# Kernel tuning notes

Hardware: AMD Instinct MI355X
Metric: run time of the kernel (lower is better)

## Reference

```python
import jax, jax.numpy as jnp
import numpy as np

BATCH = 8192
HIDDEN = 512
VOCAB = 128
SEQ_LEN = 128  # loop runs SEQ_LEN - 1 steps


def setup_inputs() -> dict:
    key = jax.random.key(0)
    ks = jax.random.split(key, 9)
    s_ih = 1.0 / np.sqrt(HIDDEN)
    inp = {
        "z": jax.random.normal(ks[0], (BATCH, HIDDEN), dtype=jnp.float32),
        # nn.LSTMCell params (gate order: i, f, g, o)
        "W_ih": jax.random.uniform(ks[1], (4 * HIDDEN, VOCAB), jnp.float32, -s_ih, s_ih),
        "W_hh": jax.random.uniform(ks[2], (4 * HIDDEN, HIDDEN), jnp.float32, -s_ih, s_ih),
        "b_ih": jax.random.uniform(ks[3], (4 * HIDDEN,), jnp.float32, -s_ih, s_ih),
        "b_hh": jax.random.uniform(ks[4], (4 * HIDDEN,), jnp.float32, -s_ih, s_ih),
        # cell_state_from_z: Linear(hidden, hidden)
        "W_cz": jax.random.uniform(ks[5], (HIDDEN, HIDDEN), jnp.float32, -s_ih, s_ih),
        "b_cz": jax.random.uniform(ks[6], (HIDDEN,), jnp.float32, -s_ih, s_ih),
        # fc: Linear(hidden, vocab)
        "W_fc": jax.random.uniform(ks[7], (VOCAB, HIDDEN), jnp.float32, -s_ih, s_ih),
        "b_fc": jax.random.uniform(ks[8], (VOCAB,), jnp.float32, -s_ih, s_ih),
    }
    return inp


def reference(z, W_ih, W_hh, b_ih, b_hh, W_cz, b_cz, W_fc, b_fc):
    batch = z.shape[0]
    # learnable cell state from z
    c0 = jax.nn.relu(z @ W_cz.T + b_cz)
    h0 = z
    # start token: one-hot at index 0
    tok0 = jnp.zeros((batch, VOCAB), dtype=z.dtype).at[:, 0].set(1.0)
    b = b_ih + b_hh

    def step(carry, _):
        h, c, tok = carry
        gates = tok @ W_ih.T + h @ W_hh.T + b  # (batch, 4H)
        i, f, g, o = jnp.split(gates, 4, axis=-1)
        i = jax.nn.sigmoid(i)
        f = jax.nn.sigmoid(f)
        g = jnp.tanh(g)
        o = jax.nn.sigmoid(o)
        c_new = f * c + i * g
        h_new = o * jnp.tanh(c_new)
        logits = jax.nn.relu(h_new @ W_fc.T + b_fc)  # (batch, vocab)
        # softmax then argmax == argmax of logits; feed one-hot of greedy token
        tok_new = jax.nn.one_hot(jnp.argmax(logits, axis=-1), VOCAB, dtype=z.dtype)
        return (h_new, c_new, tok_new), logits

    _, out = jax.lax.scan(step, (h0, c0, tok0), None, length=SEQ_LEN - 1)
    return jnp.transpose(out, (1, 0, 2))  # (batch, seq_len-1, vocab)
```

## Files before the change

### kernel.cpp

```cpp
#include <hip/hip_runtime.h>
#include <math.h>
#include <stdint.h>

#define BATCH  8192
#define HIDDEN 512
#define VOCAB  128
#define NSTEP  127
#define OUTROW (NSTEP * VOCAB)
#define NG     2048

using half8   = __attribute__((ext_vector_type(8))) _Float16;
using half4   = __attribute__((ext_vector_type(4))) _Float16;
using float4v = __attribute__((ext_vector_type(4))) float;

#define GLD16(g, l) __builtin_amdgcn_global_load_lds( \
    (const __attribute__((address_space(1))) void*)(g), \
    (__attribute__((address_space(3))) void*)(l), 16, 0, 0)

__device__ __forceinline__ float fast_rcp(float x) { return __builtin_amdgcn_rcpf(x); }
__device__ __forceinline__ float fast_sig(float x) { return fast_rcp(1.0f + __expf(-x)); }
__device__ __forceinline__ float fast_tanh(float x) { return 1.0f - 2.0f * fast_rcp(1.0f + __expf(2.0f * x)); }

__device__ __forceinline__ int orig_row_of(int np) {
    int bn = np >> 7, cc = np & 127;
    int wv = cc >> 6, cw = cc & 63;
    int gate = cw >> 4, jjl = cw & 15;
    int jj = bn * 32 + wv * 16 + jjl;
    return gate * HIDDEN + jj;
}

__global__ __launch_bounds__(256) void init_tok_kernel(int* __restrict__ tok) {
    int i = blockIdx.x * 256 + threadIdx.x;
    if (i < BATCH) tok[i] = 0;
}

__global__ __launch_bounds__(256) void prep_whh_kernel(
    const float* __restrict__ Whh, _Float16* __restrict__ wh, _Float16* __restrict__ wl)
{
    int np = blockIdx.x;
    int orig = orig_row_of(np);
    for (int k = threadIdx.x; k < HIDDEN; k += 256) {
        float w = Whh[(size_t)orig * HIDDEN + k] * 2048.0f;
        _Float16 h = (_Float16)w;
        wh[(size_t)np * HIDDEN + k] = h;
        wl[(size_t)np * HIDDEN + k] = (_Float16)(w - (float)h);
    }
}

__global__ __launch_bounds__(128) void prep_wih_kernel(
    const float* __restrict__ Wih, const float* __restrict__ bih,
    const float* __restrict__ bhh, float* __restrict__ wihT, float* __restrict__ bcomb)
{
    int np = blockIdx.x;
    int orig = orig_row_of(np);
    int v = threadIdx.x;
    wihT[(size_t)v * NG + np] = Wih[(size_t)orig * VOCAB + v];
    if (v == 0) bcomb[np] = bih[orig] + bhh[orig];
}

__global__ __launch_bounds__(256) void prep_wfc_kernel(
    const float* __restrict__ Wfc, _Float16* __restrict__ wh, _Float16* __restrict__ wl)
{
    int i = blockIdx.x * 256 + threadIdx.x;
    float w = Wfc[i] * 2048.0f;
    _Float16 h = (_Float16)w;
    wh[i] = h;
    wl[i] = (_Float16)(w - (float)h);
}

__global__ __launch_bounds__(256) void prep_z_kernel(
    const float* __restrict__ z, _Float16* __restrict__ zh, _Float16* __restrict__ zl)
{
    int i = blockIdx.x * 256 + threadIdx.x;
    float4 v = ((const float4*)z)[i];
    float s0 = v.x * 2048.f, s1 = v.y * 2048.f, s2 = v.z * 2048.f, s3 = v.w * 2048.f;
    _Float16 h0 = (_Float16)s0, h1 = (_Float16)s1, h2 = (_Float16)s2, h3 = (_Float16)s3;
    half4 H = {h0, h1, h2, h3};
    half4 L = {(_Float16)(s0 - (float)h0), (_Float16)(s1 - (float)h1),
               (_Float16)(s2 - (float)h2), (_Float16)(s3 - (float)h3)};
    ((half4*)zh)[i] = H;
    ((half4*)zl)[i] = L;
}

__global__ __launch_bounds__(256) void c0_kernel(
    const float* __restrict__ z, const float* __restrict__ Wcz,
    const float* __restrict__ bcz, float* __restrict__ c)
{
    __shared__ float As[16][128];
    __shared__ float Bs[16][128];
    const int m0 = blockIdx.x * 128;
    const int n0 = blockIdx.y * 128;
    const int tid = threadIdx.x;
    const int ty = tid >> 4, tx = tid & 15;

    float acc[8][8];
#pragma unroll
    for (int i = 0; i < 8; ++i)
#pragma unroll
        for (int j = 0; j < 8; ++j) acc[i][j] = 0.f;

    for (int kc = 0; kc < HIDDEN; kc += 16) {
#pragma unroll
        for (int i = 0; i < 2; ++i) {
            int id = tid * 2 + i;
            int row = id >> 2;
            int kq = (id & 3) * 4;
            float4 av = *(const float4*)(z + (size_t)(m0 + row) * HIDDEN + kc + kq);
            As[kq + 0][row] = av.x; As[kq + 1][row] = av.y;
            As[kq + 2][row] = av.z; As[kq + 3][row] = av.w;
            float4 bv = *(const float4*)(Wcz + (size_t)(n0 + row) * HIDDEN + kc + kq);
            Bs[kq + 0][row] = bv.x; Bs[kq + 1][row] = bv.y;
            Bs[kq + 2][row] = bv.z; Bs[kq + 3][row] = bv.w;
        }
        __syncthreads();
#pragma unroll 4
        for (int k = 0; k < 16; ++k) {
            float a[8], b[8];
            *(float4*)&a[0] = *(const float4*)&As[k][ty * 8];
            *(float4*)&a[4] = *(const float4*)&As[k][ty * 8 + 4];
            *(float4*)&b[0] = *(const float4*)&Bs[k][tx * 8];
            *(float4*)&b[4] = *(const float4*)&Bs[k][tx * 8 + 4];
#pragma unroll
            for (int i = 0; i < 8; ++i)
#pragma unroll
                for (int j = 0; j < 8; ++j)
                    acc[i][j] = fmaf(a[i], b[j], acc[i][j]);
        }
        __syncthreads();
    }
#pragma unroll
    for (int i = 0; i < 8; ++i) {
        int m = m0 + ty * 8 + i;
#pragma unroll
        for (int j = 0; j < 8; ++j) {
            int n = n0 + tx * 8 + j;
            c[(size_t)m * HIDDEN + n] = fmaxf(acc[i][j] + bcz[n], 0.f);
        }
    }
}

__global__ __launch_bounds__(512, 2) void lstm_mfma_kernel(
    const _Float16* __restrict__ hin_h, const _Float16* __restrict__ hin_l,
    const _Float16* __restrict__ whh_h, const _Float16* __restrict__ whh_l,
    const float* __restrict__ wihT, const float* __restrict__ bcomb,
    const int* __restrict__ tok, float* __restrict__ c,
    _Float16* __restrict__ hout_h, _Float16* __restrict__ hout_l)
{
    __shared__ _Float16 Ah_s[2][256][32];
    __shared__ _Float16 Al_s[2][256][32];
    __shared__ _Float16 Bh_s[2][256][32];
    __shared__ _Float16 Bl_s[2][256][32];

    const int tid  = threadIdx.x;
    const int wid  = tid >> 6, lane = tid & 63;
    const int wr   = wid >> 2, wc = wid & 3;
    const int m0   = blockIdx.x * 256;
    const int n0   = blockIdx.y * 256;

    float4v acc[8][4];
#pragma unroll
    for (int i = 0; i < 8; ++i)
#pragma unroll
        for (int j = 0; j < 4; ++j) acc[i][j] = (float4v){0.f, 0.f, 0.f, 0.f};

    const int lrow = lane >> 2;
    const int lchk = (lane & 3) ^ ((lane >> 3) & 3);
    const int loff = lrow * HIDDEN + lchk * 8;
    const int base = wid * 32;

    const _Float16* agh = hin_h + (size_t)(m0 + base) * HIDDEN + loff;
    const _Float16* agl = hin_l + (size_t)(m0 + base) * HIDDEN + loff;
    const _Float16* bgh = whh_h + (size_t)(n0 + base) * HIDDEN + loff;
    const _Float16* bgl = whh_l + (size_t)(n0 + base) * HIDDEN + loff;

    auto STAGE = [&](int buf, int kc) {
        GLD16(agh + kc,               &Ah_s[buf][base][0]);
        GLD16(agh + kc + 16 * HIDDEN, &Ah_s[buf][base + 16][0]);
        GLD16(agl + kc,               &Al_s[buf][base][0]);
        GLD16(agl + kc + 16 * HIDDEN, &Al_s[buf][base + 16][0]);
        GLD16(bgh + kc,               &Bh_s[buf][base][0]);
        GLD16(bgh + kc + 16 * HIDDEN, &Bh_s[buf][base + 16][0]);
        GLD16(bgl + kc,               &Bl_s[buf][base][0]);
        GLD16(bgl + kc + 16 * HIDDEN, &Bl_s[buf][base + 16][0]);
    };

    const int t = lane & 15, qr = lane >> 4;
    const int qa = (qr ^ ((t >> 1) & 3)) * 8;

    STAGE(0, 0);
    for (int k = 0; k < 16; ++k) {
        const int cur = k & 1;
        if (k < 15) STAGE(cur ^ 1, (k + 1) * 32);
        if (k < 15) { asm volatile("s_waitcnt vmcnt(8)" ::: "memory"); }
        else        { asm volatile("s_waitcnt vmcnt(0)" ::: "memory"); }
        __builtin_amdgcn_s_barrier();
        __builtin_amdgcn_sched_barrier(0);

        {
            const _Float16 (*AhC)[32] = Ah_s[cur];
            const _Float16 (*AlC)[32] = Al_s[cur];
            const _Float16 (*BhC)[32] = Bh_s[cur];
            const _Float16 (*BlC)[32] = Bl_s[cur];
            half8 bh[4], bl[4];
#pragma unroll
            for (int j = 0; j < 4; ++j) {
                bh[j] = *(const half8*)&BhC[wc * 64 + j * 16 + t][qa];
                bl[j] = *(const half8*)&BlC[wc * 64 + j * 16 + t][qa];
            }
#pragma unroll
            for (int i = 0; i < 8; ++i) {
                half8 ah = *(const half8*)&AhC[wr * 128 + i * 16 + t][qa];
                half8 al = *(const half8*)&AlC[wr * 128 + i * 16 + t][qa];
#pragma unroll
                for (int j = 0; j < 4; ++j) {
                    acc[i][j] = __builtin_amdgcn_mfma_f32_16x16x32_f16(ah, bh[j], acc[i][j], 0, 0, 0);
                    acc[i][j] = __builtin_amdgcn_mfma_f32_16x16x32_f16(ah, bl[j], acc[i][j], 0, 0, 0);
                    acc[i][j] = __builtin_amdgcn_mfma_f32_16x16x32_f16(al, bh[j], acc[i][j], 0, 0, 0);
                }
            }
        }
        __builtin_amdgcn_sched_barrier(0);
        if (k < 15) {
            asm volatile("" ::: "memory");
            __builtin_amdgcn_s_barrier();
        }
    }

    const float INV22 = 1.0f / 4194304.0f;
    const int g  = blockIdx.y * 4 + wc;
    const int jj = (g >> 1) * 32 + (g & 1) * 16 + t;
    const int colb = n0 + wc * 64 + t;
    float bias[4];
    int   col[4];
#pragma unroll
    for (int j = 0; j < 4; ++j) {
        col[j]  = colb + j * 16;
        bias[j] = bcomb[col[j]];
    }
#pragma unroll
    for (int i = 0; i < 8; ++i) {
        int mb = m0 + wr * 128 + i * 16 + qr * 4;
#pragma unroll
        for (int r = 0; r < 4; ++r) {
            int m  = mb + r;
            int tk = tok[m];
            const float* wv = wihT + (size_t)tk * NG;
            float iv = acc[i][0][r] * INV22 + bias[0] + wv[col[0]];
            float fv = acc[i][1][r] * INV22 + bias[1] + wv[col[1]];
            float gv = acc[i][2][r] * INV22 + bias[2] + wv[col[2]];
            float ov = acc[i][3][r] * INV22 + bias[3] + wv[col[3]];
            float ig = fast_sig(iv);
            float fg = fast_sig(fv);
            float gg = fast_tanh(gv);
            float og = fast_sig(ov);
            size_t ci = (size_t)m * HIDDEN + jj;
            float cn = fg * c[ci] + ig * gg;
            c[ci] = cn;
            float hn = og * fast_tanh(cn);
            float hs = hn * 2048.f;
            _Float16 hh = (_Float16)hs;
            hout_h[ci] = hh;
            hout_l[ci] = (_Float16)(hs - (float)hh);
        }
    }
}

__global__ __launch_bounds__(128) void logits_mfma_kernel(
    const _Float16* __restrict__ hh_, const _Float16* __restrict__ hl_,
    const _Float16* __restrict__ wfc_h, const _Float16* __restrict__ wfc_l,
    const float* __restrict__ b_fc, float* __restrict__ out_t, int* __restrict__ tok)
{
    __shared__ _Float16 Ah[32][64];
    __shared__ _Float16 Al[32][64];
    __shared__ _Float16 Bh[128][64];
    __shared__ _Float16 Bl[128][64];

    const int tid = threadIdx.x;
    const int wid = tid >> 6, lane = tid & 63;
    const int m0  = blockIdx.x * 32;
    const int t   = lane & 15, qr = lane >> 4;

    float4v acc[8];
#pragma unroll
    for (int j = 0; j < 8; ++j) acc[j] = (float4v){0.f, 0.f, 0.f, 0.f};

    const int lrow = lane >> 3;
    const int lchk = (lane & 7) ^ lrow;
    const int loff = lrow * HIDDEN + lchk * 8;

    const _Float16* Ag = (wid == 0 ? hh_ : hl_) + (size_t)m0 * HIDDEN + loff;
    _Float16* Adst = (wid == 0) ? &Ah[0][0] : &Al[0][0];
    const _Float16* Bgh = wfc_h + (size_t)(wid * 64) * HIDDEN + loff;
    const _Float16* Bgl = wfc_l + (size_t)(wid * 64) * HIDDEN + loff;

    const int sa = t & 7;

    for (int kc = 0; kc < HIDDEN; kc += 64) {
#pragma unroll
        for (int s = 0; s < 4; ++s)
            GLD16(Ag + kc + s * 8 * HIDDEN, Adst + (s * 8) * 64);
#pragma unroll
        for (int s = 0; s < 8; ++s) {
            GLD16(Bgh + kc + s * 8 * HIDDEN, &Bh[wid * 64 + s * 8][0]);
            GLD16(Bgl + kc + s * 8 * HIDDEN, &Bl[wid * 64 + s * 8][0]);
        }
        __syncthreads();
#pragma unroll
        for (int kh = 0; kh < 2; ++kh) {
            int q = kh * 4 + qr;
            int arow = wid * 16 + t;
            half8 a_h = *(const half8*)&Ah[arow][(q ^ sa) * 8];
            half8 a_l = *(const half8*)&Al[arow][(q ^ sa) * 8];
#pragma unroll
            for (int j = 0; j < 8; ++j) {
                half8 b_h = *(const half8*)&Bh[j * 16 + t][(q ^ sa) * 8];
                half8 b_l = *(const half8*)&Bl[j * 16 + t][(q ^ sa) * 8];
                acc[j] = __builtin_amdgcn_mfma_f32_16x16x32_f16(a_h, b_h, acc[j], 0, 0, 0);
                acc[j] = __builtin_amdgcn_mfma_f32_16x16x32_f16(a_h, b_l, acc[j], 0, 0, 0);
                acc[j] = __builtin_amdgcn_mfma_f32_16x16x32_f16(a_l, b_h, acc[j], 0, 0, 0);
            }
        }
        __syncthreads();
    }

    const float INV22 = 1.0f / 4194304.0f;
    float bv[8];
#pragma unroll
    for (int j = 0; j < 8; ++j) bv[j] = b_fc[j * 16 + t];

#pragma unroll
    for (int r = 0; r < 4; ++r) {
        int m = m0 + wid * 16 + qr * 4 + r;
        float vals[8];
        float vbest = -1.0f; int ibest = 0;
#pragma unroll
        for (int j = 0; j < 8; ++j) {
            float x = fmaxf(acc[j][r] * INV22 + bv[j], 0.f);
            vals[j] = x;
            if (x > vbest) { vbest = x; ibest = j * 16 + t; }
        }
        float* op = out_t + (size_t)m * OUTROW;
#pragma unroll
        for (int j = 0; j < 8; ++j) op[j * 16 + t] = vals[j];
#pragma unroll
        for (int d = 1; d < 16; d <<= 1) {
            float vo = __shfl_xor(vbest, d, 64);
            int   io = __shfl_xor(ibest, d, 64);
            if (vo > vbest || (vo == vbest && io < ibest)) { vbest = vo; ibest = io; }
        }
        if (t == 0) tok[m] = ibest;
    }
}

extern "C" void kernel_launch(void* const* d_in, const int* in_sizes, int n_in,
                              void* d_out, int out_size, void* d_ws, size_t ws_size,
                              hipStream_t stream)
{
    const float* z    = (const float*)d_in[0];
    const float* W_ih = (const float*)d_in[1];
    const float* W_hh = (const float*)d_in[2];
    const float* b_ih = (const float*)d_in[3];
    const float* b_hh = (const float*)d_in[4];
    const float* W_cz = (const float*)d_in[5];
    const float* b_cz = (const float*)d_in[6];
    const float* W_fc = (const float*)d_in[7];
    const float* b_fc = (const float*)d_in[8];
    float* out = (float*)d_out;

    uint8_t* p = (uint8_t*)d_ws;
    float* c = (float*)p;            p += (size_t)BATCH * HIDDEN * 4;
    _Float16* sA_h = (_Float16*)p;   p += (size_t)BATCH * HIDDEN * 2;
    _Float16* sA_l = (_Float16*)p;   p += (size_t)BATCH * HIDDEN * 2;
    _Float16* sB_h = (_Float16*)p;   p += (size_t)BATCH * HIDDEN * 2;
    _Float16* sB_l = (_Float16*)p;   p += (size_t)BATCH * HIDDEN * 2;
    _Float16* whhh = (_Float16*)p;   p += (size_t)NG * HIDDEN * 2;
    _Float16* whhl = (_Float16*)p;   p += (size_t)NG * HIDDEN * 2;
    _Float16* wfch = (_Float16*)p;   p += (size_t)VOCAB * HIDDEN * 2;
    _Float16* wfcl = (_Float16*)p;   p += (size_t)VOCAB * HIDDEN * 2;
    float* wihT  = (float*)p;        p += (size_t)VOCAB * NG * 4;
    float* bcomb = (float*)p;        p += (size_t)NG * 4;
    int* tokp    = (int*)p;          p += (size_t)BATCH * 4;

    init_tok_kernel<<<BATCH / 256, 256, 0, stream>>>(tokp);
    prep_whh_kernel<<<NG, 256, 0, stream>>>(W_hh, whhh, whhl);
    prep_wih_kernel<<<NG, 128, 0, stream>>>(W_ih, b_ih, b_hh, wihT, bcomb);
    prep_wfc_kernel<<<(VOCAB * HIDDEN) / 256, 256, 0, stream>>>(W_fc, wfch, wfcl);
    prep_z_kernel<<<(BATCH * HIDDEN / 4) / 256, 256, 0, stream>>>(z, sA_h, sA_l);
    c0_kernel<<<dim3(BATCH / 128, HIDDEN / 128), 256, 0, stream>>>(z, W_cz, b_cz, c);

    for (int t = 0; t < NSTEP; ++t) {
        const _Float16* inh = (t & 1) ? sB_h : sA_h;
        const _Float16* inl = (t & 1) ? sB_l : sA_l;
        _Float16* outh = (t & 1) ? sA_h : sB_h;
        _Float16* outl = (t & 1) ? sA_l : sB_l;
        lstm_mfma_kernel<<<dim3(BATCH / 256, NG / 256), 512, 0, stream>>>(
            inh, inl, whhh, whhl, wihT, bcomb, tokp, c, outh, outl);
        logits_mfma_kernel<<<BATCH / 32, 128, 0, stream>>>(
            outh, outl, wfch, wfcl, b_fc, out + (size_t)t * VOCAB, tokp);
    }
}
```

Measured before the change: 8.833 ms.

## Triple-buffer logits kernel loads and split vocab columns across four waves

The logits kernel moves from 2 to 4 waves per block. Each wave now computes a 32-row by 32-vocab tile, where before each wave did 16 rows by all 128 vocab columns. K-chunk loads go into three LDS buffers, prefetched two chunks ahead using explicit vmcnt waits and raw barriers, so global loads overlap MFMA work. The argmax becomes a two-level reduction: a shuffle within each wave, then a pass through shared memory. The cost is more LDS per block, which may lower occupancy, and hand-tuned waitcnt values that must exactly match the number of loads issued.

```diff
diff --git a/kernel.cpp b/kernel.cpp
--- a/kernel.cpp
+++ b/kernel.cpp
@@ -265,90 +265,123 @@
     }
 }
 
-__global__ __launch_bounds__(128) void logits_mfma_kernel(
+__global__ __launch_bounds__(256) void logits_mfma_kernel(
     const _Float16* __restrict__ hh_, const _Float16* __restrict__ hl_,
     const _Float16* __restrict__ wfc_h, const _Float16* __restrict__ wfc_l,
     const float* __restrict__ b_fc, float* __restrict__ out_t, int* __restrict__ tok)
 {
-    __shared__ _Float16 Ah[32][64];
-    __shared__ _Float16 Al[32][64];
-    __shared__ _Float16 Bh[128][64];
-    __shared__ _Float16 Bl[128][64];
+    __shared__ _Float16 Ah[3][32][64];
+    __shared__ _Float16 Al[3][32][64];
+    __shared__ _Float16 Bh[3][128][64];
+    __shared__ _Float16 Bl[3][128][64];
+    __shared__ float red_v[32][4];
+    __shared__ int   red_i[32][4];
 
     const int tid = threadIdx.x;
-    const int wid = tid >> 6, lane = tid & 63;
+    const int w   = tid >> 6, lane = tid & 63;
     const int m0  = blockIdx.x * 32;
     const int t   = lane & 15, qr = lane >> 4;
-
-    float4v acc[8];
-#pragma unroll
-    for (int j = 0; j < 8; ++j) acc[j] = (float4v){0.f, 0.f, 0.f, 0.f};
+    const int sa  = t & 7;
+
+    float4v acc[2][2];
+#pragma unroll
+    for (int rt = 0; rt < 2; ++rt)
+#pragma unroll
+        for (int ct = 0; ct < 2; ++ct) acc[rt][ct] = (float4v){0.f, 0.f, 0.f, 0.f};
 
     const int lrow = lane >> 3;
     const int lchk = (lane & 7) ^ lrow;
     const int loff = lrow * HIDDEN + lchk * 8;
 
-    const _Float16* Ag = (wid == 0 ? hh_ : hl_) + (size_t)m0 * HIDDEN + loff;
-    _Float16* Adst = (wid == 0) ? &Ah[0][0] : &Al[0][0];
-    const _Float16* Bgh = wfc_h + (size_t)(wid * 64) * HIDDEN + loff;
-    const _Float16* Bgl = wfc_l + (size_t)(wid * 64) * HIDDEN + loff;
-
-    const int sa = t & 7;
-
-    for (int kc = 0; kc < HIDDEN; kc += 64) {
-#pragma unroll
-        for (int s = 0; s < 4; ++s)
-            GLD16(Ag + kc + s * 8 * HIDDEN, Adst + (s * 8) * 64);
-#pragma unroll
-        for (int s = 0; s < 8; ++s) {
-            GLD16(Bgh + kc + s * 8 * HIDDEN, &Bh[wid * 64 + s * 8][0]);
-            GLD16(Bgl + kc + s * 8 * HIDDEN, &Bl[wid * 64 + s * 8][0]);
-        }
-        __syncthreads();
+    const _Float16* Agh = hh_   + (size_t)(m0 + w * 8) * HIDDEN + loff;
+    const _Float16* Agl = hl_   + (size_t)(m0 + w * 8) * HIDDEN + loff;
+    const _Float16* Bgh = wfc_h + (size_t)(w * 32) * HIDDEN + loff;
+    const _Float16* Bgl = wfc_l + (size_t)(w * 32) * HIDDEN + loff;
+
+    auto STAGE = [&](int buf, int kc) {
+        GLD16(Agh + kc, &Ah[buf][w * 8][0]);
+        GLD16(Agl + kc, &Al[buf][w * 8][0]);
+#pragma unroll
+        for (int s = 0; s < 4; ++s) {
+            GLD16(Bgh + kc + s * 8 * HIDDEN, &Bh[buf][w * 32 + s * 8][0]);
+            GLD16(Bgl + kc + s * 8 * HIDDEN, &Bl[buf][w * 32 + s * 8][0]);
+        }
+    };
+
+    STAGE(0, 0);
+    STAGE(1, 64);
+    for (int k = 0; k < 8; ++k) {
+        const int cur = k % 3;
+        __builtin_amdgcn_s_barrier();
+        if (k + 2 < 8) STAGE((k + 2) % 3, (k + 2) * 64);
+        if (k <= 5)      { asm volatile("s_waitcnt vmcnt(20)" ::: "memory"); }
+        else if (k == 6) { asm volatile("s_waitcnt vmcnt(10)" ::: "memory"); }
+        else             { asm volatile("s_waitcnt vmcnt(0)"  ::: "memory"); }
+        __builtin_amdgcn_s_barrier();
+        __builtin_amdgcn_sched_barrier(0);
+
 #pragma unroll
         for (int kh = 0; kh < 2; ++kh) {
-            int q = kh * 4 + qr;
-            int arow = wid * 16 + t;
-            half8 a_h = *(const half8*)&Ah[arow][(q ^ sa) * 8];
-            half8 a_l = *(const half8*)&Al[arow][(q ^ sa) * 8];
-#pragma unroll
-            for (int j = 0; j < 8; ++j) {
-                half8 b_h = *(const half8*)&Bh[j * 16 + t][(q ^ sa) * 8];
-                half8 b_l = *(const half8*)&Bl[j * 16 + t][(q ^ sa) * 8];
-                acc[j] = __builtin_amdgcn_mfma_f32_16x16x32_f16(a_h, b_h, acc[j], 0, 0, 0);
-                acc[j] = __builtin_amdgcn_mfma_f32_16x16x32_f16(a_h, b_l, acc[j], 0, 0, 0);
-                acc[j] = __builtin_amdgcn_mfma_f32_16x16x32_f16(a_l, b_h, acc[j], 0, 0, 0);
-            }
-        }
-        __syncthreads();
+            const int qo = ((kh * 4 + qr) ^ sa) * 8;
+            half8 a_h[2], a_l[2];
+#pragma unroll
+            for (int rt = 0; rt < 2; ++rt) {
+                a_h[rt] = *(const half8*)&Ah[cur][rt * 16 + t][qo];
+                a_l[rt] = *(const half8*)&Al[cur][rt * 16 + t][qo];
+            }
+#pragma unroll
+            for (int ct = 0; ct < 2; ++ct) {
+                half8 b_h = *(const half8*)&Bh[cur][w * 32 + ct * 16 + t][qo];
+                half8 b_l = *(const half8*)&Bl[cur][w * 32 + ct * 16 + t][qo];
+#pragma unroll
+                for (int rt = 0; rt < 2; ++rt) {
+                    acc[rt][ct] = __builtin_amdgcn_mfma_f32_16x16x32_f16(a_h[rt], b_h, acc[rt][ct], 0, 0, 0);
+                    acc[rt][ct] = __builtin_amdgcn_mfma_f32_16x16x32_f16(a_h[rt], b_l, acc[rt][ct], 0, 0, 0);
+                    acc[rt][ct] = __builtin_amdgcn_mfma_f32_16x16x32_f16(a_l[rt], b_h, acc[rt][ct], 0, 0, 0);
+                }
+            }
+        }
+        __builtin_amdgcn_sched_barrier(0);
     }
 
     const float INV22 = 1.0f / 4194304.0f;
-    float bv[8];
-#pragma unroll
-    for (int j = 0; j < 8; ++j) bv[j] = b_fc[j * 16 + t];
-
-#pragma unroll
-    for (int r = 0; r < 4; ++r) {
-        int m = m0 + wid * 16 + qr * 4 + r;
-        float vals[8];
-        float vbest = -1.0f; int ibest = 0;
-#pragma unroll
-        for (int j = 0; j < 8; ++j) {
-            float x = fmaxf(acc[j][r] * INV22 + bv[j], 0.f);
-            vals[j] = x;
-            if (x > vbest) { vbest = x; ibest = j * 16 + t; }
-        }
-        float* op = out_t + (size_t)m * OUTROW;
-#pragma unroll
-        for (int j = 0; j < 8; ++j) op[j * 16 + t] = vals[j];
-#pragma unroll
-        for (int d = 1; d < 16; d <<= 1) {
-            float vo = __shfl_xor(vbest, d, 64);
-            int   io = __shfl_xor(ibest, d, 64);
-            if (vo > vbest || (vo == vbest && io < ibest)) { vbest = vo; ibest = io; }
-        }
-        if (t == 0) tok[m] = ibest;
+    float bv[2];
+    bv[0] = b_fc[w * 32 + t];
+    bv[1] = b_fc[w * 32 + 16 + t];
+
+#pragma unroll
+    for (int rt = 0; rt < 2; ++rt) {
+#pragma unroll
+        for (int r = 0; r < 4; ++r) {
+            const int rl = rt * 16 + qr * 4 + r;
+            const int m  = m0 + rl;
+            float vbest = -1.0f; int ibest = 0;
+            float* op = out_t + (size_t)m * OUTROW + w * 32;
+#pragma unroll
+            for (int ct = 0; ct < 2; ++ct) {
+                float x = fmaxf(acc[rt][ct][r] * INV22 + bv[ct], 0.f);
+                op[ct * 16 + t] = x;
+                int idx = w * 32 + ct * 16 + t;
+                if (x > vbest) { vbest = x; ibest = idx; }
+            }
+#pragma unroll
+            for (int d = 1; d < 16; d <<= 1) {
+                float vo = __shfl_xor(vbest, d, 64);
+                int   io = __shfl_xor(ibest, d, 64);
+                if (vo > vbest || (vo == vbest && io < ibest)) { vbest = vo; ibest = io; }
+            }
+            if (t == 0) { red_v[rl][w] = vbest; red_i[rl][w] = ibest; }
+        }
+    }
+    __syncthreads();
+    if (tid < 32) {
+        float vbest = red_v[tid][0]; int ibest = red_i[tid][0];
+#pragma unroll
+        for (int ww = 1; ww < 4; ++ww) {
+            float v = red_v[tid][ww]; int i2 = red_i[tid][ww];
+            if (v > vbest || (v == vbest && i2 < ibest)) { vbest = v; ibest = i2; }
+        }
+        tok[m0 + tid] = ibest;
     }
 }
 
@@ -395,7 +428,7 @@
         _Float16* outl = (t & 1) ? sA_l : sB_l;
         lstm_mfma_kernel<<<dim3(BATCH / 256, NG / 256), 512, 0, stream>>>(
             inh, inl, whhh, whhl, wihT, bcomb, tokp, c, outh, outl);
-        logits_mfma_kernel<<<BATCH / 32, 128, 0, stream>>>(
+        logits_mfma_kernel<<<BATCH / 32, 256, 0, stream>>>(
             outh, outl, wfch, wfcl, b_fc, out + (size_t)t * VOCAB, tokp);
     }
 }
```

Result: faster. 8.630 ms (-2.3%).
